# Performance work log

Hardware: AMD Instinct MI355X
Metric: run time of the kernel (lower is better)

## Reference

```python
import jax, jax.numpy as jnp
import numpy as np

N_NODES = 50000
N_EDGES = 600000
CH = 128


def _mlp(h, w1, b1, w2, b2):
    # Linear -> ReLU -> Linear (weights stored [in, out])
    return jax.nn.relu(h @ w1 + b1) @ w2 + b2


def setup_inputs() -> dict:
    key = jax.random.key(0)
    ks = jax.random.split(key, 12)
    def lin(k, fan_in, fan_out):
        bound = 1.0 / np.sqrt(fan_in)
        kw, kb = jax.random.split(k)
        w = jax.random.uniform(kw, (fan_in, fan_out), jnp.float32, -bound, bound)
        b = jax.random.uniform(kb, (fan_out,), jnp.float32, -bound, bound)
        return w, b
    ew1, eb1 = lin(ks[0], 3 * CH, CH)
    ew2, eb2 = lin(ks[1], CH, CH)
    nw1, nb1 = lin(ks[2], 2 * CH, CH)
    nw2, nb2 = lin(ks[3], CH, CH)
    x = jax.random.normal(ks[4], (N_NODES, CH), jnp.float32)
    edge_attr = jax.random.normal(ks[5], (N_EDGES, CH), jnp.float32)
    edge_index = jax.random.randint(ks[6], (2, N_EDGES), 0, N_NODES, jnp.int64 if jax.config.read('jax_enable_x64') else jnp.int32)
    return {"x": x, "edge_index": edge_index, "edge_attr": edge_attr,
            "ew1": ew1, "eb1": eb1, "ew2": ew2, "eb2": eb2,
            "nw1": nw1, "nb1": nb1, "nw2": nw2, "nb2": nb2}


def reference(x, edge_index, edge_attr, ew1, eb1, ew2, eb2, nw1, nb1, nw2, nb2):
    row, col = edge_index[0], edge_index[1]
    n = x.shape[0]
    # edge model: concat(source, target, edge_attr) -> MLP -> new edge_attr
    e_in = jnp.concatenate([x[row], x[col], edge_attr], axis=1)  # [E, 3*ch]
    new_edge_attr = _mlp(e_in, ew1, eb1, ew2, eb2)               # [E, ch]
    # node model: concat(x[col], new_edge_attr) -> MLP -> scatter_mean over row
    n_in = jnp.concatenate([x[col], new_edge_attr], axis=1)      # [E, 2*ch]
    msg = _mlp(n_in, nw1, nb1, nw2, nb2)                         # [E, ch]
    seg_sum = jax.ops.segment_sum(msg, row, num_segments=n)      # [N, ch]
    cnt = jax.ops.segment_sum(jnp.ones((msg.shape[0],), msg.dtype), row, num_segments=n)
    new_x = seg_sum / jnp.maximum(cnt, 1.0)[:, None]             # scatter_mean
    return new_x, new_edge_attr
```

## Files before the change

### kernel.cpp

```cpp
#include <hip/hip_runtime.h>
#include <stdint.h>

#define NN 50000
#define NE 600000
#define CH 128
#define RT 2
#define EPB 128

typedef __attribute__((ext_vector_type(8))) short short8;
typedef __attribute__((ext_vector_type(4))) float f32x4;
typedef __attribute__((ext_vector_type(4))) uint32_t u32x4;

__device__ __forceinline__ ushort f2bf(float f) {
  union { float f; uint32_t u; } v; v.f = f;
  uint32_t u = v.u;
  return (ushort)((u + 0x7FFFu + ((u >> 16) & 1u)) >> 16);
}
__device__ __forceinline__ float bf2f(uint32_t u16) {
  union { uint32_t u; float f; } t; t.u = u16 << 16; return t.f;
}
__device__ __forceinline__ uint32_t cvtpk_bf16(float a, float b) {
  uint32_t r;
  asm("v_cvt_pk_bf16_f32 %0, %1, %2" : "=v"(r) : "v"(a), "v"(b));
  return r;
}

__global__ void prep_frag_k(const float* __restrict__ ew1, const float* __restrict__ ew2,
                            const float* __restrict__ nw1, const float* __restrict__ nw2,
                            ushort* __restrict__ wB) {
  int idx = blockIdx.x * 256 + threadIdx.x;
  if (idx >= 114688) return;
  const float* src; int local;
  if (idx < 49152)      { src = ew1; local = idx; }
  else if (idx < 65536) { src = ew2; local = idx - 49152; }
  else if (idx < 98304) { src = nw1; local = idx - 65536; }
  else                  { src = nw2; local = idx - 98304; }
  int ks   = local >> 12;
  int rem  = local & 4095;
  int nt   = rem >> 9;
  int t    = rem & 511;
  int lane = t >> 3, i = t & 7;
  int k = ks * 32 + (lane >> 4) * 8 + i;
  int n = nt * 16 + (lane & 15);
  wB[idx] = f2bf(src[k * 128 + n]);
}

__global__ void convert_x_k(const float* __restrict__ x, ushort* __restrict__ xb) {
  int i = blockIdx.x * 256 + threadIdx.x;
  if (i >= NN * CH / 4) return;
  const float4 f = reinterpret_cast<const float4*>(x)[i];
  ushort4 r;
  r.x = f2bf(f.x); r.y = f2bf(f.y); r.z = f2bf(f.z); r.w = f2bf(f.w);
  reinterpret_cast<ushort4*>(xb)[i] = r;
}

__global__ void rank_k(const int* __restrict__ ei, unsigned* __restrict__ cnt,
                       unsigned* __restrict__ rank) {
  int e = blockIdx.x * 256 + threadIdx.x;
  if (e < NE) rank[e] = atomicAdd(&cnt[ei[e]], 1u);
}

__global__ void scan_k(const unsigned* __restrict__ cnt, unsigned* __restrict__ start) {
  __shared__ unsigned s[1024];
  const int CHUNK = (NN + 1023) / 1024;
  int t = threadIdx.x;
  int lo = t * CHUNK, hi = lo + CHUNK < NN ? lo + CHUNK : NN;
  unsigned sum = 0;
  for (int i = lo; i < hi; ++i) sum += cnt[i];
  s[t] = sum;
  __syncthreads();
  for (int off = 1; off < 1024; off <<= 1) {
    unsigned v = (t >= off) ? s[t - off] : 0u;
    __syncthreads();
    s[t] += v;
    __syncthreads();
  }
  unsigned run = t ? s[t - 1] : 0u;
  for (int i = lo; i < hi; ++i) { start[i] = run; run += cnt[i]; }
}

__global__ void dest_k(const int* __restrict__ ei, const unsigned* __restrict__ start,
                       const unsigned* __restrict__ rank, unsigned* __restrict__ dest) {
  int e = blockIdx.x * 256 + threadIdx.x;
  if (e < NE) dest[e] = start[ei[e]] + rank[e];
}

__device__ __forceinline__ void mm8(const ushort* Bcbuf, int lane,
                                    const short8 a[RT], f32x4 acc[RT][8]) {
#pragma unroll
  for (int nt = 0; nt < 8; ++nt) {
    short8 b = *reinterpret_cast<const short8*>(Bcbuf + nt * 512 + lane * 8);
#pragma unroll
    for (int rt = 0; rt < RT; ++rt)
      acc[rt][nt] = __builtin_amdgcn_mfma_f32_16x16x32_bf16(a[rt], b, acc[rt][nt], 0, 0, 0);
  }
}

__global__ __launch_bounds__(256, 2) void fused_k(
    const int* __restrict__ ei, const float* __restrict__ edge_attr,
    const ushort* __restrict__ wB,
    const float* __restrict__ eb1, const float* __restrict__ eb2,
    const float* __restrict__ nb1, const float* __restrict__ nb2,
    const ushort* __restrict__ xb, const unsigned* __restrict__ dest,
    ushort* __restrict__ msg, float* __restrict__ out_e)
{
  __shared__ ushort hbuf[4][RT * 16][136];
  __shared__ ushort Bc[4][4096];
  const int tid  = threadIdx.x;
  const int lane = tid & 63;
  const int widx = tid >> 6;
  const int wbase = blockIdx.x * EPB + widx * (RT * 16);
  const int l15 = lane & 15;
  const int g = lane >> 4;
  const int kg = g * 8;
  ushort (*h)[136] = hbuf[widx];

  short8 bt[2][4];

#define LDB2(set, ph) do { \
    const ushort* _s = wB + (size_t)(ph) * 4096 + tid * 16; \
    bt[set][0] = *reinterpret_cast<const short8*>(_s); \
    bt[set][1] = *reinterpret_cast<const short8*>(_s + 8); \
    bt[set][2] = *reinterpret_cast<const short8*>(_s + 4096); \
    bt[set][3] = *reinterpret_cast<const short8*>(_s + 4096 + 8); \
  } while (0)
#define STB2(set, ph) do { \
    ushort* _d0 = &Bc[(ph) & 3][tid * 16]; \
    ushort* _d1 = &Bc[((ph) + 1) & 3][tid * 16]; \
    *reinterpret_cast<short8*>(_d0)     = bt[set][0]; \
    *reinterpret_cast<short8*>(_d0 + 8) = bt[set][1]; \
    *reinterpret_cast<short8*>(_d1)     = bt[set][2]; \
    *reinterpret_cast<short8*>(_d1 + 8) = bt[set][3]; \
  } while (0)
#define BAR() do { \
    asm volatile("s_waitcnt lgkmcnt(0)" ::: "memory"); \
    __builtin_amdgcn_s_barrier(); \
  } while (0)
#define STEP(s, A0, A1, DO_LDB, DO_STB, DO_BAR) do { \
    __builtin_amdgcn_s_setprio(1); \
    mm8(Bc[(2 * (s)) & 3], lane, A0, acc); \
    mm8(Bc[(2 * (s) + 1) & 3], lane, A1, acc); \
    __builtin_amdgcn_s_setprio(0); \
    if (DO_LDB) LDB2((s) & 1, 2 * (s) + 4); \
    if (DO_STB) STB2(((s) + 1) & 1, 2 * (s) + 2); \
    if (DO_BAR) BAR(); \
  } while (0)
#define LDH(dst, ksl) do { \
    _Pragma("unroll") \
    for (int _rt = 0; _rt < RT; ++_rt) \
      dst[_rt] = *reinterpret_cast<const short8*>(&h[_rt * 16 + l15][(ksl) * 32 + kg]); \
  } while (0)

  LDB2(0, 0);
  LDB2(1, 2);

  int rowA[RT], colA[RT], eAc[RT];
#pragma unroll
  for (int rt = 0; rt < RT; ++rt) {
    int e = wbase + rt * 16 + l15;
    eAc[rt] = e < NE ? e : NE - 1;
    rowA[rt] = ei[eAc[rt]];
    colA[rt] = ei[NE + eAc[rt]];
  }
  short8 axr[4][RT], axc[4][RT];
#pragma unroll
  for (int ksl = 0; ksl < 4; ++ksl)
#pragma unroll
    for (int rt = 0; rt < RT; ++rt) {
      axr[ksl][rt] = *reinterpret_cast<const short8*>(xb + rowA[rt] * CH + ksl * 32 + kg);
      axc[ksl][rt] = *reinterpret_cast<const short8*>(xb + colA[rt] * CH + ksl * 32 + kg);
    }
  short8 eab[4][RT];
#pragma unroll
  for (int ksl = 0; ksl < 4; ++ksl)
#pragma unroll
    for (int rt = 0; rt < RT; ++rt) {
      const float* pp = edge_attr + (size_t)eAc[rt] * CH + ksl * 32 + kg;
      float4 f0 = *reinterpret_cast<const float4*>(pp);
      float4 f1 = *reinterpret_cast<const float4*>(pp + 4);
      union { u32x4 u; short8 s; } cv;
      cv.u = (u32x4){ cvtpk_bf16(f0.x, f0.y), cvtpk_bf16(f0.z, f0.w),
                      cvtpk_bf16(f1.x, f1.y), cvtpk_bf16(f1.z, f1.w) };
      eab[ksl][rt] = cv.s;
    }
  unsigned dp[RT * 4];
#pragma unroll
  for (int it = 0; it < RT * 4; ++it) {
    int er = wbase + it * 4 + g;
    dp[it] = dest[er < NE ? er : NE - 1];
  }

  STB2(0, 0);
  BAR();

  const f32x4 zero4 = {0.f, 0.f, 0.f, 0.f};
  f32x4 acc[RT][8];
  short8 ha0[RT], ha1[RT];

#pragma unroll
  for (int rt = 0; rt < RT; ++rt)
#pragma unroll
    for (int nt = 0; nt < 8; ++nt) acc[rt][nt] = zero4;

  STEP(0, axr[0], axr[1], 1, 1, 1);
  STEP(1, axr[2], axr[3], 1, 1, 1);
  STEP(2, axc[0], axc[1], 1, 1, 1);
  STEP(3, axc[2], axc[3], 1, 1, 1);
  STEP(4, eab[0], eab[1], 1, 1, 1);
  STEP(5, eab[2], eab[3], 1, 1, 1);
#pragma unroll
  for (int nt = 0; nt < 8; ++nt) {
    float bb = eb1[nt * 16 + l15];
#pragma unroll
    for (int rt = 0; rt < RT; ++rt)
#pragma unroll
      for (int r = 0; r < 4; r += 2) {
        float v0 = fmaxf(acc[rt][nt][r] + bb, 0.f);
        float v1 = fmaxf(acc[rt][nt][r + 1] + bb, 0.f);
        uint32_t pk = cvtpk_bf16(v0, v1);
        h[rt * 16 + g * 4 + r][nt * 16 + l15]     = (ushort)(pk & 0xffffu);
        h[rt * 16 + g * 4 + r + 1][nt * 16 + l15] = (ushort)(pk >> 16);
      }
  }

#pragma unroll
  for (int rt = 0; rt < RT; ++rt)
#pragma unroll
    for (int nt = 0; nt < 8; ++nt) acc[rt][nt] = zero4;
  LDH(ha0, 0); LDH(ha1, 1);
  STEP(6, ha0, ha1, 1, 1, 1);
  LDH(ha0, 2); LDH(ha1, 3);
  STEP(7, ha0, ha1, 1, 1, 1);
#pragma unroll
  for (int nt = 0; nt < 8; ++nt) {
    float bb = eb2[nt * 16 + l15];
#pragma unroll
    for (int rt = 0; rt < RT; ++rt) {
      float v[4];
#pragma unroll
      for (int r = 0; r < 4; ++r) {
        v[r] = acc[rt][nt][r] + bb;
        int erow = wbase + rt * 16 + g * 4 + r;
        if (erow < NE) out_e[(size_t)erow * CH + nt * 16 + l15] = v[r];
      }
#pragma unroll
      for (int r = 0; r < 4; r += 2) {
        uint32_t pk = cvtpk_bf16(v[r], v[r + 1]);
        h[rt * 16 + g * 4 + r][nt * 16 + l15]     = (ushort)(pk & 0xffffu);
        h[rt * 16 + g * 4 + r + 1][nt * 16 + l15] = (ushort)(pk >> 16);
      }
    }
  }

#pragma unroll
  for (int rt = 0; rt < RT; ++rt)
#pragma unroll
    for (int nt = 0; nt < 8; ++nt) acc[rt][nt] = zero4;
  STEP(8, axc[0], axc[1], 1, 1, 1);
  STEP(9, axc[2], axc[3], 1, 1, 1);
  LDH(ha0, 0); LDH(ha1, 1);
  STEP(10, ha0, ha1, 1, 1, 1);
  LDH(ha0, 2); LDH(ha1, 3);
  STEP(11, ha0, ha1, 1, 1, 1);
#pragma unroll
  for (int nt = 0; nt < 8; ++nt) {
    float bb = nb1[nt * 16 + l15];
#pragma unroll
    for (int rt = 0; rt < RT; ++rt)
#pragma unroll
      for (int r = 0; r < 4; r += 2) {
        float v0 = fmaxf(acc[rt][nt][r] + bb, 0.f);
        float v1 = fmaxf(acc[rt][nt][r + 1] + bb, 0.f);
        uint32_t pk = cvtpk_bf16(v0, v1);
        h[rt * 16 + g * 4 + r][nt * 16 + l15]     = (ushort)(pk & 0xffffu);
        h[rt * 16 + g * 4 + r + 1][nt * 16 + l15] = (ushort)(pk >> 16);
      }
  }

#pragma unroll
  for (int rt = 0; rt < RT; ++rt)
#pragma unroll
    for (int nt = 0; nt < 8; ++nt) acc[rt][nt] = zero4;
  LDH(ha0, 0); LDH(ha1, 1);
  STEP(12, ha0, ha1, 0, 1, 1);
  LDH(ha0, 2); LDH(ha1, 3);
  STEP(13, ha0, ha1, 0, 0, 0);
#pragma unroll
  for (int nt = 0; nt < 8; ++nt) {
    float bb = nb2[nt * 16 + l15];
#pragma unroll
    for (int rt = 0; rt < RT; ++rt)
#pragma unroll
      for (int r = 0; r < 4; r += 2) {
        uint32_t pk = cvtpk_bf16(acc[rt][nt][r] + bb, acc[rt][nt][r + 1] + bb);
        h[rt * 16 + g * 4 + r][nt * 16 + l15]     = (ushort)(pk & 0xffffu);
        h[rt * 16 + g * 4 + r + 1][nt * 16 + l15] = (ushort)(pk >> 16);
      }
  }
#pragma unroll
  for (int it = 0; it < RT * 4; ++it) {
    int row = it * 4 + g;
    int er = wbase + row;
    int col = l15 * 8;
    short8 v = *reinterpret_cast<const short8*>(&h[row][col]);
    if (er < NE)
      *reinterpret_cast<short8*>(msg + (size_t)dp[it] * CH + col) = v;
  }
#undef LDB2
#undef STB2
#undef BAR
#undef STEP
#undef LDH
}

__global__ __launch_bounds__(256) void reduce_k(const ushort* __restrict__ msg,
    const unsigned* __restrict__ cnt, const unsigned* __restrict__ start,
    float* __restrict__ out_x) {
  int w = blockIdx.x * 4 + (threadIdx.x >> 6);
  if (w >= NN) return;
  int lane = threadIdx.x & 63;
  unsigned deg = cnt[w], s = start[w];
  float a0 = 0.f, a1 = 0.f;
#pragma unroll 4
  for (unsigned j = 0; j < deg; ++j) {
    uint32_t pk = *reinterpret_cast<const uint32_t*>(msg + (size_t)(s + j) * CH + lane * 2);
    a0 += bf2f(pk & 0xffffu);
    a1 += bf2f(pk >> 16);
  }
  float inv = 1.0f / fmaxf((float)deg, 1.0f);
  float2 o; o.x = a0 * inv; o.y = a1 * inv;
  *reinterpret_cast<float2*>(out_x + (size_t)w * CH + lane * 2) = o;
}

extern "C" void kernel_launch(void* const* d_in, const int* in_sizes, int n_in,
                              void* d_out, int out_size, void* d_ws, size_t ws_size,
                              hipStream_t stream) {
  const float* x   = (const float*)d_in[0];
  const int*   ei  = (const int*)d_in[1];
  const float* ea  = (const float*)d_in[2];
  const float* ew1 = (const float*)d_in[3];
  const float* eb1 = (const float*)d_in[4];
  const float* ew2 = (const float*)d_in[5];
  const float* eb2 = (const float*)d_in[6];
  const float* nw1 = (const float*)d_in[7];
  const float* nb1 = (const float*)d_in[8];
  const float* nw2 = (const float*)d_in[9];
  const float* nb2 = (const float*)d_in[10];

  float* out_x = (float*)d_out;
  float* out_e = (float*)d_out + (size_t)NN * CH;

  char* wsb = (char*)d_ws;
  ushort*   msg    = (ushort*)wsb;
  ushort*   wB     = (ushort*)(wsb + 153600000);
  ushort*   xb     = (ushort*)(wsb + 153829376);
  unsigned* cnt    = (unsigned*)(wsb + 166629376);
  unsigned* start  = (unsigned*)(wsb + 166829376);
  unsigned* rank   = (unsigned*)(wsb + 167029376);
  unsigned* dest   = (unsigned*)(wsb + 169429376);

  hipMemsetAsync(cnt, 0, (size_t)NN * sizeof(unsigned), stream);

  prep_frag_k<<<448, 256, 0, stream>>>(ew1, ew2, nw1, nw2, wB);
  convert_x_k<<<(NN * CH / 4 + 255) / 256, 256, 0, stream>>>(x, xb);
  rank_k<<<(NE + 255) / 256, 256, 0, stream>>>(ei, cnt, rank);
  scan_k<<<1, 1024, 0, stream>>>(cnt, start);
  dest_k<<<(NE + 255) / 256, 256, 0, stream>>>(ei, start, rank, dest);

  int nblk = (NE + EPB - 1) / EPB;
  fused_k<<<nblk, 256, 0, stream>>>(ei, ea, wB, eb1, eb2, nb1, nb2, xb, dest, msg, out_e);

  reduce_k<<<(NN + 3) / 4, 256, 0, stream>>>(msg, cnt, start, out_x);
}
```

Before: 434.7 us.

## Merge prep kernels into one launch and parallelize the prefix scan

Combines the weight-fragment prep, x-to-bf16 conversion and per-edge rank atomics into a single kernel with block-range dispatch, which removes two launches. It also replaces the single-block serial-chunk scan over node counts with a three-phase multi-block scan (block reductions, scan of partials, per-block scan). The old scan ran on one CU with sequential chunk loops, so parallelizing it targets that serialized latency. In exchange it adds two small launches and a new workspace buffer for the partials.

```diff
diff --git a/kernel.cpp b/kernel.cpp
--- a/kernel.cpp
+++ b/kernel.cpp
@@ -6,6 +6,7 @@
 #define CH 128
 #define RT 2
 #define EPB 128
+#define NPART 196
 
 typedef __attribute__((ext_vector_type(8))) short short8;
 typedef __attribute__((ext_vector_type(4))) float f32x4;
@@ -25,58 +26,86 @@
   return r;
 }
 
-__global__ void prep_frag_k(const float* __restrict__ ew1, const float* __restrict__ ew2,
-                            const float* __restrict__ nw1, const float* __restrict__ nw2,
-                            ushort* __restrict__ wB) {
-  int idx = blockIdx.x * 256 + threadIdx.x;
-  if (idx >= 114688) return;
-  const float* src; int local;
-  if (idx < 49152)      { src = ew1; local = idx; }
-  else if (idx < 65536) { src = ew2; local = idx - 49152; }
-  else if (idx < 98304) { src = nw1; local = idx - 65536; }
-  else                  { src = nw2; local = idx - 98304; }
-  int ks   = local >> 12;
-  int rem  = local & 4095;
-  int nt   = rem >> 9;
-  int t    = rem & 511;
-  int lane = t >> 3, i = t & 7;
-  int k = ks * 32 + (lane >> 4) * 8 + i;
-  int n = nt * 16 + (lane & 15);
-  wB[idx] = f2bf(src[k * 128 + n]);
-}
-
-__global__ void convert_x_k(const float* __restrict__ x, ushort* __restrict__ xb) {
-  int i = blockIdx.x * 256 + threadIdx.x;
-  if (i >= NN * CH / 4) return;
-  const float4 f = reinterpret_cast<const float4*>(x)[i];
-  ushort4 r;
-  r.x = f2bf(f.x); r.y = f2bf(f.y); r.z = f2bf(f.z); r.w = f2bf(f.w);
-  reinterpret_cast<ushort4*>(xb)[i] = r;
-}
-
-__global__ void rank_k(const int* __restrict__ ei, unsigned* __restrict__ cnt,
-                       unsigned* __restrict__ rank) {
-  int e = blockIdx.x * 256 + threadIdx.x;
-  if (e < NE) rank[e] = atomicAdd(&cnt[ei[e]], 1u);
-}
-
-__global__ void scan_k(const unsigned* __restrict__ cnt, unsigned* __restrict__ start) {
-  __shared__ unsigned s[1024];
-  const int CHUNK = (NN + 1023) / 1024;
+__global__ void prep_all_k(const float* __restrict__ ew1, const float* __restrict__ ew2,
+                           const float* __restrict__ nw1, const float* __restrict__ nw2,
+                           ushort* __restrict__ wB,
+                           const float* __restrict__ x, ushort* __restrict__ xb,
+                           const int* __restrict__ ei, unsigned* __restrict__ cnt,
+                           unsigned* __restrict__ rank) {
+  int b = blockIdx.x, tid = threadIdx.x;
+  if (b < 448) {
+    int idx = b * 256 + tid;
+    const float* src; int local;
+    if (idx < 49152)      { src = ew1; local = idx; }
+    else if (idx < 65536) { src = ew2; local = idx - 49152; }
+    else if (idx < 98304) { src = nw1; local = idx - 65536; }
+    else                  { src = nw2; local = idx - 98304; }
+    int ks   = local >> 12;
+    int rem  = local & 4095;
+    int nt   = rem >> 9;
+    int t    = rem & 511;
+    int lane = t >> 3, i = t & 7;
+    int k = ks * 32 + (lane >> 4) * 8 + i;
+    int n = nt * 16 + (lane & 15);
+    wB[idx] = f2bf(src[k * 128 + n]);
+  } else if (b < 6698) {
+    int i = (b - 448) * 256 + tid;
+    const float4 f = reinterpret_cast<const float4*>(x)[i];
+    ushort4 r;
+    r.x = f2bf(f.x); r.y = f2bf(f.y); r.z = f2bf(f.z); r.w = f2bf(f.w);
+    reinterpret_cast<ushort4*>(xb)[i] = r;
+  } else {
+    int e = (b - 6698) * 256 + tid;
+    if (e < NE) rank[e] = atomicAdd(&cnt[ei[e]], 1u);
+  }
+}
+
+__global__ void scan1_k(const unsigned* __restrict__ cnt, unsigned* __restrict__ part) {
+  __shared__ unsigned s[256];
   int t = threadIdx.x;
-  int lo = t * CHUNK, hi = lo + CHUNK < NN ? lo + CHUNK : NN;
-  unsigned sum = 0;
-  for (int i = lo; i < hi; ++i) sum += cnt[i];
-  s[t] = sum;
+  int i = blockIdx.x * 256 + t;
+  s[t] = i < NN ? cnt[i] : 0u;
   __syncthreads();
-  for (int off = 1; off < 1024; off <<= 1) {
-    unsigned v = (t >= off) ? s[t - off] : 0u;
+#pragma unroll
+  for (int off = 128; off > 0; off >>= 1) {
+    if (t < off) s[t] += s[t + off];
     __syncthreads();
-    s[t] += v;
+  }
+  if (t == 0) part[blockIdx.x] = s[0];
+}
+
+__global__ void scan2_k(unsigned* __restrict__ part) {
+  __shared__ unsigned s[256];
+  int t = threadIdx.x;
+  unsigned v = t < NPART ? part[t] : 0u;
+  s[t] = v;
+  __syncthreads();
+#pragma unroll
+  for (int off = 1; off < 256; off <<= 1) {
+    unsigned u = (t >= off) ? s[t - off] : 0u;
     __syncthreads();
-  }
-  unsigned run = t ? s[t - 1] : 0u;
-  for (int i = lo; i < hi; ++i) { start[i] = run; run += cnt[i]; }
+    s[t] += u;
+    __syncthreads();
+  }
+  if (t < NPART) part[t] = s[t] - v;
+}
+
+__global__ void scan3_k(const unsigned* __restrict__ cnt, const unsigned* __restrict__ part,
+                        unsigned* __restrict__ start) {
+  __shared__ unsigned s[256];
+  int t = threadIdx.x;
+  int i = blockIdx.x * 256 + t;
+  unsigned v = i < NN ? cnt[i] : 0u;
+  s[t] = v;
+  __syncthreads();
+#pragma unroll
+  for (int off = 1; off < 256; off <<= 1) {
+    unsigned u = (t >= off) ? s[t - off] : 0u;
+    __syncthreads();
+    s[t] += u;
+    __syncthreads();
+  }
+  if (i < NN) start[i] = part[blockIdx.x] + s[t] - v;
 }
 
 __global__ void dest_k(const int* __restrict__ ei, const unsigned* __restrict__ start,
@@ -358,13 +387,14 @@
   unsigned* start  = (unsigned*)(wsb + 166829376);
   unsigned* rank   = (unsigned*)(wsb + 167029376);
   unsigned* dest   = (unsigned*)(wsb + 169429376);
+  unsigned* part   = (unsigned*)(wsb + 171829376);
 
   hipMemsetAsync(cnt, 0, (size_t)NN * sizeof(unsigned), stream);
 
-  prep_frag_k<<<448, 256, 0, stream>>>(ew1, ew2, nw1, nw2, wB);
-  convert_x_k<<<(NN * CH / 4 + 255) / 256, 256, 0, stream>>>(x, xb);
-  rank_k<<<(NE + 255) / 256, 256, 0, stream>>>(ei, cnt, rank);
-  scan_k<<<1, 1024, 0, stream>>>(cnt, start);
+  prep_all_k<<<9042, 256, 0, stream>>>(ew1, ew2, nw1, nw2, wB, x, xb, ei, cnt, rank);
+  scan1_k<<<NPART, 256, 0, stream>>>(cnt, part);
+  scan2_k<<<1, 256, 0, stream>>>(part);
+  scan3_k<<<NPART, 256, 0, stream>>>(cnt, part, start);
   dest_k<<<(NE + 255) / 256, 256, 0, stream>>>(ei, start, rank, dest);
 
   int nblk = (NE + EPB - 1) / EPB;
```

Measured after the change: 361.7 us, median of 2. 16.8% less time.
